# Kernel tuning notes

Hardware: AMD Instinct MI355X
Metric: run time of the kernel (lower is better)

## Reference

```python
import jax, jax.numpy as jnp
import numpy as np

# Grid spacing (CartesianGrid3D.dx / .dy)
DX = 1000.0
DY = 1000.0
WENO_EPS = 1e-6  # classic Jiang-Shu smoothness regularizer

NZ, NY, NX = 32, 1024, 1024


def _weno5_recon(qm2, qm1, q0, qp1, qp2):
    """Classic WENO5 (Jiang-Shu) reconstruction of q at the i+1/2 face,
    left-biased (stencil centered on cell i)."""
    c1312 = 13.0 / 12.0
    b0 = c1312 * (qm2 - 2.0 * qm1 + q0) ** 2 + 0.25 * (qm2 - 4.0 * qm1 + 3.0 * q0) ** 2
    b1 = c1312 * (qm1 - 2.0 * q0 + qp1) ** 2 + 0.25 * (qm1 - qp1) ** 2
    b2 = c1312 * (q0 - 2.0 * qp1 + qp2) ** 2 + 0.25 * (3.0 * q0 - 4.0 * qp1 + qp2) ** 2
    a0 = 0.1 / (WENO_EPS + b0) ** 2
    a1 = 0.6 / (WENO_EPS + b1) ** 2
    a2 = 0.3 / (WENO_EPS + b2) ** 2
    p0 = (2.0 * qm2 - 7.0 * qm1 + 11.0 * q0) / 6.0
    p1 = (-qm1 + 5.0 * q0 + 2.0 * qp1) / 6.0
    p2 = (2.0 * q0 + 5.0 * qp1 - qp2) / 6.0
    return (a0 * p0 + a1 * p1 + a2 * p2) / (a0 + a1 + a2)


def _weno5_flux(q, vel, axis):
    """Upwinded WENO5 flux vel * q_face at face i+1/2 along `axis`.
    Edge-padded so the flux array has the same shape as q (faithful to
    recon.weno5_x / weno5_y producing full-shape flux arrays whose interior
    is consumed by the divergence)."""
    q = jnp.moveaxis(q, axis, -1)
    vel = jnp.moveaxis(vel, axis, -1)
    n = q.shape[-1]
    pad = [(0, 0)] * (q.ndim - 1) + [(2, 3)]
    qp = jnp.pad(q, pad, mode='edge')
    sl = lambda o: qp[..., o:o + n]
    qm2, qm1, q0, qp1, qp2, qp3 = sl(0), sl(1), sl(2), sl(3), sl(4), sl(5)
    q_left = _weno5_recon(qm2, qm1, q0, qp1, qp2)          # upwind for vel >= 0
    q_right = _weno5_recon(qp3, qp2, qp1, q0, qm1)         # mirrored, vel < 0
    f = vel * jnp.where(vel >= 0.0, q_left, q_right)
    return jnp.moveaxis(f, -1, axis)


def setup_inputs() -> dict:
    key = jax.random.key(0)
    kh, ku, kv = jax.random.split(key, 3)
    h = jax.random.normal(kh, (NZ, NY, NX), dtype=jnp.float32)
    u = jax.random.normal(ku, (NZ, NY, NX), dtype=jnp.float32)
    v = jax.random.normal(kv, (NZ, NY, NX), dtype=jnp.float32)
    return {"h": h, "u": u, "v": v}


def reference(h, u, v):
    # fe: flux through east face (x), fn: flux through north face (y)
    fe = _weno5_flux(h, u, axis=2)
    fn = _weno5_flux(h, v, axis=1)
    div = ((fe[1:-1, 2:-2, 2:-2] - fe[1:-1, 2:-2, 1:-3]) / DX
           + (fn[1:-1, 2:-2, 2:-2] - fn[1:-1, 1:-3, 2:-2]) / DY)
    out = jnp.zeros_like(h)
    out = out.at[1:-1, 2:-2, 2:-2].set(-div)
    return out
```

## Files before the change

### kernel.cpp

```cpp
#include <hip/hip_runtime.h>

#define NZ 32
#define NY 1024
#define NX 1024
#define TY 8

__device__ __forceinline__ float rcpf(float x) { return __builtin_amdgcn_rcpf(x); }

__device__ __forceinline__ float weno5(float qm2, float qm1, float q0, float qp1, float qp2) {
    const float c1312 = 13.0f / 12.0f;
    float t0 = qm2 - 2.0f * qm1 + q0;
    float u0 = qm2 - 4.0f * qm1 + 3.0f * q0;
    float b0 = c1312 * t0 * t0 + 0.25f * u0 * u0;
    float t1 = qm1 - 2.0f * q0 + qp1;
    float u1 = qm1 - qp1;
    float b1 = c1312 * t1 * t1 + 0.25f * u1 * u1;
    float t2 = q0 - 2.0f * qp1 + qp2;
    float u2 = 3.0f * q0 - 4.0f * qp1 + qp2;
    float b2 = c1312 * t2 * t2 + 0.25f * u2 * u2;
    float e0 = 1e-6f + b0, e1 = 1e-6f + b1, e2 = 1e-6f + b2;
    float s0 = e0 * e0, s1 = e1 * e1, s2 = e2 * e2;
    float a0 = 0.1f * (s1 * s2);
    float a1 = 0.6f * (s0 * s2);
    float a2 = 0.3f * (s0 * s1);
    float p0 = (1.0f / 3.0f) * qm2 + (-7.0f / 6.0f) * qm1 + (11.0f / 6.0f) * q0;
    float p1 = (-1.0f / 6.0f) * qm1 + (5.0f / 6.0f) * q0 + (1.0f / 3.0f) * qp1;
    float p2 = (1.0f / 3.0f) * q0 + (5.0f / 6.0f) * qp1 + (-1.0f / 6.0f) * qp2;
    return (a0 * p0 + a1 * p1 + a2 * p2) * rcpf(a0 + a1 + a2);
}

__device__ __forceinline__ float upwind_flux(float vel, float qm2, float qm1, float q0,
                                             float qp1, float qp2, float qp3) {
    bool up = vel >= 0.0f;
    float s0 = up ? qm2 : qp3;
    float s1 = up ? qm1 : qp2;
    float s2 = up ? q0  : qp1;
    float s3 = up ? qp1 : q0;
    float s4 = up ? qp2 : qm1;
    return vel * weno5(s0, s1, s2, s3, s4);
}

__global__ __launch_bounds__(256) void adv_kernel(const float* __restrict__ h,
                                                  const float* __restrict__ u,
                                                  const float* __restrict__ v,
                                                  float* __restrict__ out) {
    const int tid = threadIdx.x;
    const int px  = blockIdx.x * 256 + tid;
    const int x0  = px * 2;
    const int z   = blockIdx.z;
    const int y0  = blockIdx.y * TY;
    const size_t zoff = (size_t)z * (NY * NX);
    const float* __restrict__ hz = h + zoff;
    const float* __restrict__ uz = u + zoff;
    const float* __restrict__ vz = v + zoff;
    float* __restrict__ oz = out + zoff;

    if (z == 0 || z == NZ - 1) {
#pragma unroll
        for (int t = 0; t < TY; ++t)
            *(float2*)(oz + (y0 + t) * NX + x0) = make_float2(0.0f, 0.0f);
        return;
    }

    const bool xfast = (x0 >= 4) && (x0 <= NX - 6);
    const bool xint  = (px >= 1) && (px <= (NX - 4) / 2);
    const bool lane0 = (tid & 63) == 0;

    float2 hy[7];
#pragma unroll
    for (int k = 0; k < 7; ++k) {
        int yy = y0 - 3 + k;
        yy = yy < 0 ? 0 : (yy > NY - 1 ? NY - 1 : yy);
        hy[k] = *(const float2*)(hz + yy * NX + x0);
    }

    const int ym1 = (y0 > 0) ? y0 - 1 : 0;
    float2 vm = *(const float2*)(vz + ym1 * NX + x0);
    float fn_lo_e = upwind_flux(vm.x, hy[0].x, hy[1].x, hy[2].x, hy[3].x, hy[4].x, hy[5].x);
    float fn_lo_o = upwind_flux(vm.y, hy[0].y, hy[1].y, hy[2].y, hy[3].y, hy[4].y, hy[5].y);

#pragma unroll
    for (int t = 0; t < TY; ++t) {
        const int y   = y0 + t;
        const int row = y * NX;
        const float* __restrict__ rp  = hz + row;
        const float* __restrict__ rpu = uz + row;

        float sl[10];
        if (xfast) {
            float2 m2  = *(const float2*)(rp + x0 - 4);
            float2 m1  = *(const float2*)(rp + x0 - 2);
            float2 pp1 = *(const float2*)(rp + x0 + 2);
            float2 pp2 = *(const float2*)(rp + x0 + 4);
            sl[0] = m2.x;  sl[1] = m2.y;
            sl[2] = m1.x;  sl[3] = m1.y;
            sl[6] = pp1.x; sl[7] = pp1.y;
            sl[8] = pp2.x; sl[9] = pp2.y;
        } else {
#pragma unroll
            for (int k = 0; k < 10; ++k) {
                if (k == 4 || k == 5) continue;
                int xx = x0 - 4 + k;
                xx = xx < 0 ? 0 : (xx > NX - 1 ? NX - 1 : xx);
                sl[k] = rp[xx];
            }
        }
        sl[4] = hy[3].x;
        sl[5] = hy[3].y;

        float2 uv = *(const float2*)(rpu + x0);
        float2 vv = *(const float2*)(vz + row + x0);

        float f_e = upwind_flux(uv.x, sl[2], sl[3], sl[4], sl[5], sl[6], sl[7]);
        float f_o = upwind_flux(uv.y, sl[3], sl[4], sl[5], sl[6], sl[7], sl[8]);

        float fe_lo = __shfl_up(f_o, 1);
        if (lane0) {
            int xm = x0 - 1;
            xm = xm < 0 ? 0 : xm;
            fe_lo = upwind_flux(rpu[xm], sl[1], sl[2], sl[3], sl[4], sl[5], sl[6]);
        }

        float fn_e = upwind_flux(vv.x, hy[1].x, hy[2].x, hy[3].x, hy[4].x, hy[5].x, hy[6].x);
        float fn_o = upwind_flux(vv.y, hy[1].y, hy[2].y, hy[3].y, hy[4].y, hy[5].y, hy[6].y);

        const float inv_d = 1.0f / 1000.0f;
        bool yin = (y >= 2) && (y <= NY - 3);
        bool wr  = xint && yin;
        float2 res;
        res.x = wr ? -((f_e - fe_lo) + (fn_e - fn_lo_e)) * inv_d : 0.0f;
        res.y = wr ? -((f_o - f_e) + (fn_o - fn_lo_o)) * inv_d : 0.0f;
        *(float2*)(oz + row + x0) = res;

        fn_lo_e = fn_e;
        fn_lo_o = fn_o;
#pragma unroll
        for (int k = 0; k < 6; ++k) hy[k] = hy[k + 1];
        int yn = y + 4;
        yn = yn > NY - 1 ? NY - 1 : yn;
        hy[6] = *(const float2*)(hz + yn * NX + x0);
    }
}

extern "C" void kernel_launch(void* const* d_in, const int* in_sizes, int n_in,
                              void* d_out, int out_size, void* d_ws, size_t ws_size,
                              hipStream_t stream) {
    const float* h = (const float*)d_in[0];
    const float* u = (const float*)d_in[1];
    const float* v = (const float*)d_in[2];
    float* out = (float*)d_out;

    dim3 block(256, 1, 1);
    dim3 grid(NX / 512, NY / TY, NZ);
    adv_kernel<<<grid, block, 0, stream>>>(h, u, v, out);
}
```

Measured before the change: 396.6 us.

## Process four x-points per thread with float4 loads and double row tile

Each thread now computes four adjacent x outputs using float4 loads instead of two with float2. The x-face flux on the left is recomputed locally rather than taken through a wavefront shuffle with a lane-0 fallback, so the lane-0 divergence goes away. The y tile grows from 8 to 16 rows, which cuts the redundant halo loads and the initial y-flux recomputation per block. The costs are more registers, fewer blocks (a grid of 1x64x32), and the loop being only partially unrolled.

```diff
diff --git a/kernel.cpp b/kernel.cpp
--- a/kernel.cpp
+++ b/kernel.cpp
@@ -3,7 +3,7 @@
 #define NZ 32
 #define NY 1024
 #define NX 1024
-#define TY 8
+#define TY 16
 
 __device__ __forceinline__ float rcpf(float x) { return __builtin_amdgcn_rcpf(x); }
 
@@ -45,8 +45,7 @@
                                                   const float* __restrict__ v,
                                                   float* __restrict__ out) {
     const int tid = threadIdx.x;
-    const int px  = blockIdx.x * 256 + tid;
-    const int x0  = px * 2;
+    const int x0  = tid * 4;
     const int z   = blockIdx.z;
     const int y0  = blockIdx.y * TY;
     const size_t zoff = (size_t)z * (NY * NX);
@@ -56,89 +55,91 @@
     float* __restrict__ oz = out + zoff;
 
     if (z == 0 || z == NZ - 1) {
-#pragma unroll
+#pragma unroll 4
         for (int t = 0; t < TY; ++t)
-            *(float2*)(oz + (y0 + t) * NX + x0) = make_float2(0.0f, 0.0f);
+            *(float4*)(oz + (y0 + t) * NX + x0) = make_float4(0.f, 0.f, 0.f, 0.f);
         return;
     }
 
-    const bool xfast = (x0 >= 4) && (x0 <= NX - 6);
-    const bool xint  = (px >= 1) && (px <= (NX - 4) / 2);
-    const bool lane0 = (tid & 63) == 0;
+    const bool xin0 = (x0 + 0 >= 2) && (x0 + 0 <= NX - 3);
+    const bool xin1 = (x0 + 1 >= 2) && (x0 + 1 <= NX - 3);
+    const bool xin2 = (x0 + 2 >= 2) && (x0 + 2 <= NX - 3);
+    const bool xin3 = (x0 + 3 >= 2) && (x0 + 3 <= NX - 3);
+    const bool xfast = (x0 >= 4) && (x0 + 7 <= NX - 1);
+    const int  xm1   = x0 > 0 ? x0 - 1 : 0;
 
-    float2 hy[7];
+    float4 hy[7];
 #pragma unroll
     for (int k = 0; k < 7; ++k) {
         int yy = y0 - 3 + k;
         yy = yy < 0 ? 0 : (yy > NY - 1 ? NY - 1 : yy);
-        hy[k] = *(const float2*)(hz + yy * NX + x0);
+        hy[k] = *(const float4*)(hz + yy * NX + x0);
     }
 
     const int ym1 = (y0 > 0) ? y0 - 1 : 0;
-    float2 vm = *(const float2*)(vz + ym1 * NX + x0);
-    float fn_lo_e = upwind_flux(vm.x, hy[0].x, hy[1].x, hy[2].x, hy[3].x, hy[4].x, hy[5].x);
-    float fn_lo_o = upwind_flux(vm.y, hy[0].y, hy[1].y, hy[2].y, hy[3].y, hy[4].y, hy[5].y);
+    float4 vm = *(const float4*)(vz + ym1 * NX + x0);
+    float4 fn_lo;
+    fn_lo.x = upwind_flux(vm.x, hy[0].x, hy[1].x, hy[2].x, hy[3].x, hy[4].x, hy[5].x);
+    fn_lo.y = upwind_flux(vm.y, hy[0].y, hy[1].y, hy[2].y, hy[3].y, hy[4].y, hy[5].y);
+    fn_lo.z = upwind_flux(vm.z, hy[0].z, hy[1].z, hy[2].z, hy[3].z, hy[4].z, hy[5].z);
+    fn_lo.w = upwind_flux(vm.w, hy[0].w, hy[1].w, hy[2].w, hy[3].w, hy[4].w, hy[5].w);
 
-#pragma unroll
+#pragma unroll 4
     for (int t = 0; t < TY; ++t) {
         const int y   = y0 + t;
         const int row = y * NX;
         const float* __restrict__ rp  = hz + row;
         const float* __restrict__ rpu = uz + row;
 
-        float sl[10];
+        float s0, s1, s2, s3, s8, s9, s10;
         if (xfast) {
-            float2 m2  = *(const float2*)(rp + x0 - 4);
-            float2 m1  = *(const float2*)(rp + x0 - 2);
-            float2 pp1 = *(const float2*)(rp + x0 + 2);
-            float2 pp2 = *(const float2*)(rp + x0 + 4);
-            sl[0] = m2.x;  sl[1] = m2.y;
-            sl[2] = m1.x;  sl[3] = m1.y;
-            sl[6] = pp1.x; sl[7] = pp1.y;
-            sl[8] = pp2.x; sl[9] = pp2.y;
+            float4 hm = *(const float4*)(rp + x0 - 4);
+            float4 hp = *(const float4*)(rp + x0 + 4);
+            s0 = hm.x; s1 = hm.y; s2 = hm.z; s3 = hm.w;
+            s8 = hp.x; s9 = hp.y; s10 = hp.z;
         } else {
-#pragma unroll
-            for (int k = 0; k < 10; ++k) {
-                if (k == 4 || k == 5) continue;
-                int xx = x0 - 4 + k;
-                xx = xx < 0 ? 0 : (xx > NX - 1 ? NX - 1 : xx);
-                sl[k] = rp[xx];
-            }
+            int i0 = x0 - 4 < 0 ? 0 : x0 - 4;
+            int i1 = x0 - 3 < 0 ? 0 : x0 - 3;
+            int i2 = x0 - 2 < 0 ? 0 : x0 - 2;
+            int i3 = x0 - 1 < 0 ? 0 : x0 - 1;
+            int i8 = x0 + 4 > NX - 1 ? NX - 1 : x0 + 4;
+            int i9 = x0 + 5 > NX - 1 ? NX - 1 : x0 + 5;
+            int ia = x0 + 6 > NX - 1 ? NX - 1 : x0 + 6;
+            s0 = rp[i0]; s1 = rp[i1]; s2 = rp[i2]; s3 = rp[i3];
+            s8 = rp[i8]; s9 = rp[i9]; s10 = rp[ia];
         }
-        sl[4] = hy[3].x;
-        sl[5] = hy[3].y;
+        const float s4 = hy[3].x, s5 = hy[3].y, s6 = hy[3].z, s7 = hy[3].w;
 
-        float2 uv = *(const float2*)(rpu + x0);
-        float2 vv = *(const float2*)(vz + row + x0);
+        float4 uu = *(const float4*)(rpu + x0);
+        float  um = rpu[xm1];
+        float4 vv = *(const float4*)(vz + row + x0);
 
-        float f_e = upwind_flux(uv.x, sl[2], sl[3], sl[4], sl[5], sl[6], sl[7]);
-        float f_o = upwind_flux(uv.y, sl[3], sl[4], sl[5], sl[6], sl[7], sl[8]);
+        float fw = upwind_flux(um,   s1, s2, s3, s4, s5, s6);
+        float f0 = upwind_flux(uu.x, s2, s3, s4, s5, s6, s7);
+        float f1 = upwind_flux(uu.y, s3, s4, s5, s6, s7, s8);
+        float f2 = upwind_flux(uu.z, s4, s5, s6, s7, s8, s9);
+        float f3 = upwind_flux(uu.w, s5, s6, s7, s8, s9, s10);
 
-        float fe_lo = __shfl_up(f_o, 1);
-        if (lane0) {
-            int xm = x0 - 1;
-            xm = xm < 0 ? 0 : xm;
-            fe_lo = upwind_flux(rpu[xm], sl[1], sl[2], sl[3], sl[4], sl[5], sl[6]);
-        }
-
-        float fn_e = upwind_flux(vv.x, hy[1].x, hy[2].x, hy[3].x, hy[4].x, hy[5].x, hy[6].x);
-        float fn_o = upwind_flux(vv.y, hy[1].y, hy[2].y, hy[3].y, hy[4].y, hy[5].y, hy[6].y);
+        float fn0 = upwind_flux(vv.x, hy[1].x, hy[2].x, hy[3].x, hy[4].x, hy[5].x, hy[6].x);
+        float fn1 = upwind_flux(vv.y, hy[1].y, hy[2].y, hy[3].y, hy[4].y, hy[5].y, hy[6].y);
+        float fn2 = upwind_flux(vv.z, hy[1].z, hy[2].z, hy[3].z, hy[4].z, hy[5].z, hy[6].z);
+        float fn3 = upwind_flux(vv.w, hy[1].w, hy[2].w, hy[3].w, hy[4].w, hy[5].w, hy[6].w);
 
         const float inv_d = 1.0f / 1000.0f;
-        bool yin = (y >= 2) && (y <= NY - 3);
-        bool wr  = xint && yin;
-        float2 res;
-        res.x = wr ? -((f_e - fe_lo) + (fn_e - fn_lo_e)) * inv_d : 0.0f;
-        res.y = wr ? -((f_o - f_e) + (fn_o - fn_lo_o)) * inv_d : 0.0f;
-        *(float2*)(oz + row + x0) = res;
+        const bool yin = (y >= 2) && (y <= NY - 3);
+        float4 res;
+        res.x = (xin0 && yin) ? -((f0 - fw) + (fn0 - fn_lo.x)) * inv_d : 0.0f;
+        res.y = (xin1 && yin) ? -((f1 - f0) + (fn1 - fn_lo.y)) * inv_d : 0.0f;
+        res.z = (xin2 && yin) ? -((f2 - f1) + (fn2 - fn_lo.z)) * inv_d : 0.0f;
+        res.w = (xin3 && yin) ? -((f3 - f2) + (fn3 - fn_lo.w)) * inv_d : 0.0f;
+        *(float4*)(oz + row + x0) = res;
 
-        fn_lo_e = fn_e;
-        fn_lo_o = fn_o;
+        fn_lo = make_float4(fn0, fn1, fn2, fn3);
 #pragma unroll
         for (int k = 0; k < 6; ++k) hy[k] = hy[k + 1];
         int yn = y + 4;
         yn = yn > NY - 1 ? NY - 1 : yn;
-        hy[6] = *(const float2*)(hz + yn * NX + x0);
+        hy[6] = *(const float4*)(hz + yn * NX + x0);
     }
 }
 
@@ -151,6 +152,6 @@
     float* out = (float*)d_out;
 
     dim3 block(256, 1, 1);
-    dim3 grid(NX / 512, NY / TY, NZ);
+    dim3 grid(1, NY / TY, NZ);
     adv_kernel<<<grid, block, 0, stream>>>(h, u, v, out);
 }
```

New measurement: 404.4 us. No clear change (+2.0%).
